# Kernel optimization log

Hardware: AMD Instinct MI355X
Metric: run time of the kernel (lower is better)

## Reference

```python
import jax, jax.numpy as jnp
import numpy as np

# ---- geometry constants (from init_kwargs options) ----
VIEWS, NDET, NX, NY = 360, 736, 512, 512
DVOX, DDET = 0.7, 1.2858
DSO, DOD = 595.0, 490.6
DSD = DSO + DOD
STEP = 0.0174533
END_ANGLE = STEP * VIEWS  # ~2*pi
EXTENT = 1


def _compute_indices():
    """CPU port of PixelIndexCal_cuda (fanflat mode, extent=1).
    Returns flat int64 indices of shape [NX*NY*VIEWS] (pixel-major, view inner)."""
    sVx, sVy = DVOX * NX, DVOX * NY
    alphas = np.linspace(0.0, END_ANGLE, VIEWS, endpoint=False)
    indX, indY = np.meshgrid(np.arange(NX, dtype=np.float64),
                             np.arange(NY, dtype=np.float64), indexing='ij')
    idx_all = np.empty((NX * NY, VIEWS), dtype=np.int64)
    for a in range(VIEWS):
        alpha = -alphas[a]
        c, s = np.cos(alpha), np.sin(alpha)
        P0x = -(sVx / 2 - DVOX / 2)
        P0y = sVy / 2 - DVOX / 2
        rot = lambda px, py: (px * c + py * s, -px * s + py * c)
        Px_, Py_ = rot(P0x, P0y)
        Pxx, Pxy = rot(P0x + DVOX, P0y)
        Pyx, Pyy = rot(P0x, P0y - DVOX)
        Py_, Pxy, Pyy = Py_ / DDET, Pxy / DDET, Pyy / DDET
        dXx, dXy = Pxx - Px_, Pxy - Py_
        dYx, dYy = Pyx - Px_, Pyy - Py_
        # per-pixel rotated coords
        Pix = Px_ + indX * dXx + indY * dYx
        Piy = Py_ + indX * dXy + indY * dYy
        # fanflat: source at (DSO, 0); ray hits detector plane at x = DSO-DSD
        vectX = Pix - DSO
        t = -DSD / vectX
        det = Piy * t + NDET / 2.0
        det = np.clip(det, 1.0, NDET - 2.0)
        idx_all[:, a] = (det + NDET * a).astype(np.int64).ravel()
    return idx_all.reshape(-1)


def _conv(x, w, b):
    y = jax.lax.conv_general_dilated(x, w, (1, 1), 'SAME',
                                     dimension_numbers=('NCHW', 'OIHW', 'NCHW'))
    return y + b[None, :, None, None]


def setup_inputs() -> dict:
    key = jax.random.key(0)
    ks = jax.random.split(key, 16)
    lin_std = 1.0 / np.sqrt(NDET)
    conv_std = 1.0 / np.sqrt(64 * 9)
    inp = {
        'x': jax.random.normal(ks[0], (1, 1, VIEWS, NDET), jnp.float32),
        'indices': jnp.asarray(_compute_indices()),
        'w1': jax.random.normal(ks[1], (NDET, NDET), jnp.float32) * lin_std,
        'b1': jnp.zeros((NDET,), jnp.float32),
        'w2': jax.random.normal(ks[2], (NDET, NDET), jnp.float32) * lin_std,
        'b2': jnp.zeros((NDET,), jnp.float32),
        'conv_in_w': jax.random.normal(ks[3], (64, 1, 3, 3), jnp.float32) * (1.0 / 3.0),
        'conv_in_b': jnp.zeros((64,), jnp.float32),
        'blk_w1': jax.random.normal(ks[4], (11, 64, 64, 3, 3), jnp.float32) * conv_std,
        'blk_b1': jnp.zeros((11, 64), jnp.float32),
        'blk_w2': jax.random.normal(ks[5], (11, 64, 64, 3, 3), jnp.float32) * conv_std,
        'blk_b2': jnp.zeros((11, 64), jnp.float32),
        'conv_out_w': jax.random.normal(ks[6], (1, 64, 3, 3), jnp.float32) * conv_std,
        'conv_out_b': jnp.zeros((1,), jnp.float32),
    }
    return inp


def reference(x, indices, w1, b1, w2, b2, conv_in_w, conv_in_b,
              blk_w1, blk_b1, blk_w2, blk_b2, conv_out_w, conv_out_b):
    # convf: two per-detector-row Linear+ReLU over last dim (nDetecU)
    h = jax.nn.relu(x @ w1.T + b1)
    h = jax.nn.relu(h @ w2.T + b2)
    # BackProjNet (learn=False): gather + sum over views, scale, flip
    sino = h.reshape(-1, 1, VIEWS * NDET)
    g = sino[:, :, indices]                         # [B,1,NX*NY*VIEWS]
    g = g.reshape(-1, 1, NX * NY, VIEWS * EXTENT)
    img = g.sum(axis=3) * ((END_ANGLE - 0.0) / (2 * VIEWS * EXTENT))
    img = img.reshape(-1, 1, NX, NY)
    img = jnp.flip(img, axis=(2, 3))
    # rCNN refinement: conv(1->64)+ReLU, 11 residual blocks, conv(64->1)
    y = jax.nn.relu(_conv(img, conv_in_w, conv_in_b))
    for i in range(11):
        z = _conv(y, blk_w1[i], blk_b1[i])
        z = jax.nn.relu(z)
        z = _conv(z, blk_w2[i], blk_b2[i])
        y = jax.nn.relu(y + z)
    out = _conv(y, conv_out_w, conv_out_b)
    return out
```

## Files before the change

kernel.cpp:

```cpp
#include <hip/hip_runtime.h>

#define VIEWS 360
#define NDET 736
#define NX 512
#define NY 512
#define NPIX (NX * NY)

typedef unsigned short u16;
typedef __attribute__((ext_vector_type(8))) short bf16x8;
typedef __attribute__((ext_vector_type(4))) float f32x4;

__device__ __forceinline__ u16 f2bf(float f) {
  unsigned u = __float_as_uint(f);
  return (u16)((u + 0x7fffu + ((u >> 16) & 1u)) >> 16);
}

__global__ __launch_bounds__(256) void linear_relu4_kernel(
    const float* __restrict__ in, const float* __restrict__ w,
    const float* __restrict__ b, float* __restrict__ out) {
  __shared__ __align__(16) float xin[4][NDET];
  const int v0 = blockIdx.x * 4;
  const int t = threadIdx.x;
  for (int k = t; k < 4 * (NDET / 4); k += 256) {
    const int row = k / (NDET / 4), c4 = k % (NDET / 4);
    ((float4*)xin[row])[c4] = ((const float4*)(in + (size_t)(v0 + row) * NDET))[c4];
  }
  __syncthreads();

  const bool has2 = (t < NDET - 512);
  const float4* w0 = (const float4*)(w + (size_t)t * NDET);
  const float4* w1 = (const float4*)(w + (size_t)(t + 256) * NDET);
  const float4* w2 = (const float4*)(w + (size_t)(has2 ? t + 512 : t) * NDET);

  float acc[3][4];
#pragma unroll
  for (int j = 0; j < 3; ++j)
#pragma unroll
    for (int v = 0; v < 4; ++v) acc[j][v] = 0.f;

#pragma unroll 2
  for (int k = 0; k < NDET / 4; ++k) {
    float4 xv0 = ((const float4*)xin[0])[k];
    float4 xv1 = ((const float4*)xin[1])[k];
    float4 xv2 = ((const float4*)xin[2])[k];
    float4 xv3 = ((const float4*)xin[3])[k];
    float4 wv;
    wv = w0[k];
    acc[0][0] = fmaf(xv0.x, wv.x, fmaf(xv0.y, wv.y, fmaf(xv0.z, wv.z, fmaf(xv0.w, wv.w, acc[0][0]))));
    acc[0][1] = fmaf(xv1.x, wv.x, fmaf(xv1.y, wv.y, fmaf(xv1.z, wv.z, fmaf(xv1.w, wv.w, acc[0][1]))));
    acc[0][2] = fmaf(xv2.x, wv.x, fmaf(xv2.y, wv.y, fmaf(xv2.z, wv.z, fmaf(xv2.w, wv.w, acc[0][2]))));
    acc[0][3] = fmaf(xv3.x, wv.x, fmaf(xv3.y, wv.y, fmaf(xv3.z, wv.z, fmaf(xv3.w, wv.w, acc[0][3]))));
    wv = w1[k];
    acc[1][0] = fmaf(xv0.x, wv.x, fmaf(xv0.y, wv.y, fmaf(xv0.z, wv.z, fmaf(xv0.w, wv.w, acc[1][0]))));
    acc[1][1] = fmaf(xv1.x, wv.x, fmaf(xv1.y, wv.y, fmaf(xv1.z, wv.z, fmaf(xv1.w, wv.w, acc[1][1]))));
    acc[1][2] = fmaf(xv2.x, wv.x, fmaf(xv2.y, wv.y, fmaf(xv2.z, wv.z, fmaf(xv2.w, wv.w, acc[1][2]))));
    acc[1][3] = fmaf(xv3.x, wv.x, fmaf(xv3.y, wv.y, fmaf(xv3.z, wv.z, fmaf(xv3.w, wv.w, acc[1][3]))));
    wv = w2[k];
    acc[2][0] = fmaf(xv0.x, wv.x, fmaf(xv0.y, wv.y, fmaf(xv0.z, wv.z, fmaf(xv0.w, wv.w, acc[2][0]))));
    acc[2][1] = fmaf(xv1.x, wv.x, fmaf(xv1.y, wv.y, fmaf(xv1.z, wv.z, fmaf(xv1.w, wv.w, acc[2][1]))));
    acc[2][2] = fmaf(xv2.x, wv.x, fmaf(xv2.y, wv.y, fmaf(xv2.z, wv.z, fmaf(xv2.w, wv.w, acc[2][2]))));
    acc[2][3] = fmaf(xv3.x, wv.x, fmaf(xv3.y, wv.y, fmaf(xv3.z, wv.z, fmaf(xv3.w, wv.w, acc[2][3]))));
  }

  const float b0 = b[t], b1 = b[t + 256];
  const float b2v = has2 ? b[t + 512] : 0.f;
#pragma unroll
  for (int v = 0; v < 4; ++v) {
    float* o = out + (size_t)(v0 + v) * NDET;
    o[t] = fmaxf(acc[0][v] + b0, 0.f);
    o[t + 256] = fmaxf(acc[1][v] + b1, 0.f);
    if (has2) o[t + 512] = fmaxf(acc[2][v] + b2v, 0.f);
  }
}

__global__ __launch_bounds__(256) void backproj_kernel(
    const float* __restrict__ sino, const int* __restrict__ idx,
    float* __restrict__ img) {
  __shared__ int lidx[256 * 77];
  const int t = threadIdx.x;
  const int p_base = blockIdx.x * 256;

  float a0 = 0.f, a1 = 0.f, a2 = 0.f, a3 = 0.f;

#pragma unroll 1
  for (int c = 0; c < 5; ++c) {
    if (c) __syncthreads();
#pragma unroll
    for (int k = 0; k < 18; ++k) {
      const int f = k * 256 + t;
      const int row = f / 18, col4 = f % 18;
      int4 v = *(const int4*)&idx[(size_t)(p_base + row) * VIEWS + c * 72 +
                                  col4 * 4];
      int* dst = &lidx[row * 77 + col4 * 4];
      dst[0] = v.x; dst[1] = v.y; dst[2] = v.z; dst[3] = v.w;
    }
    __syncthreads();
    const int* myrow = &lidx[t * 77];
#pragma unroll
    for (int j = 0; j < 72; j += 4) {
      a0 += sino[myrow[j + 0]];
      a1 += sino[myrow[j + 1]];
      a2 += sino[myrow[j + 2]];
      a3 += sino[myrow[j + 3]];
    }
  }

  const int p = p_base + t;
  const int ix = p >> 9, iy = p & 511;
  img[(NX - 1 - ix) * NY + (NY - 1 - iy)] =
      ((a0 + a1) + (a2 + a3)) * 0.00872665f;
}

__device__ __forceinline__ void load9(const float* __restrict__ base, int gx,
                                      int gy, float v[9]) {
  const bool xm = gx > 0, xp = gx < NX - 1, ym = gy > 0, yp = gy < NY - 1;
  const float* c = base + gy * NX + gx;
  v[0] = (ym && xm) ? c[-NX - 1] : 0.f;
  v[1] = (ym)       ? c[-NX]     : 0.f;
  v[2] = (ym && xp) ? c[-NX + 1] : 0.f;
  v[3] = (xm)       ? c[-1]      : 0.f;
  v[4] =               c[0];
  v[5] = (xp)       ? c[1]       : 0.f;
  v[6] = (yp && xm) ? c[NX - 1]  : 0.f;
  v[7] = (yp)       ? c[NX]      : 0.f;
  v[8] = (yp && xp) ? c[NX + 1]  : 0.f;
}

__device__ __forceinline__ float dot9(float a, const float v[9],
                                      const float* __restrict__ w) {
  a = fmaf(v[0], w[0], a);
  a = fmaf(v[1], w[1], a);
  a = fmaf(v[2], w[2], a);
  a = fmaf(v[3], w[3], a);
  a = fmaf(v[4], w[4], a);
  a = fmaf(v[5], w[5], a);
  a = fmaf(v[6], w[6], a);
  a = fmaf(v[7], w[7], a);
  a = fmaf(v[8], w[8], a);
  return a;
}

__global__ __launch_bounds__(256) void conv_in_kernel(
    const float* __restrict__ in, const float* __restrict__ w,
    const float* __restrict__ b, float* __restrict__ out) {
  const int p = blockIdx.x * 256 + threadIdx.x;
  const int gx = p & (NX - 1), gy = p >> 9;
  float v[9];
  load9(in, gx, gy, v);
  float4* o = (float4*)(out + (size_t)p * 64);
#pragma unroll
  for (int oq = 0; oq < 16; ++oq) {
    float4 r;
    r.x = fmaxf(dot9(b[oq * 4 + 0], v, w + (oq * 4 + 0) * 9), 0.f);
    r.y = fmaxf(dot9(b[oq * 4 + 1], v, w + (oq * 4 + 1) * 9), 0.f);
    r.z = fmaxf(dot9(b[oq * 4 + 2], v, w + (oq * 4 + 2) * 9), 0.f);
    r.w = fmaxf(dot9(b[oq * 4 + 3], v, w + (oq * 4 + 3) * 9), 0.f);
    o[oq] = r;
  }
}

__global__ __launch_bounds__(256) void prep_weights_kernel(
    const float* __restrict__ bw1, const float* __restrict__ bw2,
    u16* __restrict__ wR) {
  const int g = blockIdx.x * 256 + threadIdx.x;
  if (g >= 22 * 36864) return;
  const int li = g / 36864, r1 = g % 36864;
  const int s = r1 / 2048, r2 = r1 % 2048;
  const int mf = r2 / 512, r3 = r2 % 512;
  const int lane = r3 / 8, j = r3 % 8;
  const int kb = s / 9, tap = s % 9;
  const int kg = lane >> 4, n = lane & 15;
  const int oc = mf * 16 + n;
  const int ic = kb * 32 + kg * 8 + j;
  const float* src = (li < 11) ? bw1 + li * 36864 : bw2 + (li - 11) * 36864;
  wR[g] = f2bf(src[(oc * 64 + ic) * 9 + tap]);
}

template <int IN_BF, int OUT_BF, int RELU, int ADDRES>
__global__ __launch_bounds__(256, 4) void conv64_mfma(
    const void* __restrict__ in_, const u16* __restrict__ wA,
    const float* __restrict__ bias, const float* __restrict__ res,
    void* __restrict__ out_) {
  __shared__ __align__(16) u16 lds[6 * 66 * 32];
  const int xb = (blockIdx.x & 7) * 64;
  const int yb = (int)(blockIdx.x >> 3) * 4;
  const int tid = threadIdx.x;
  const int wv = tid >> 6;
  const int lane = tid & 63;
  const int n = lane & 15;
  const int kg = lane >> 4;

  f32x4 acc[4][4];
#pragma unroll
  for (int i = 0; i < 4; ++i)
#pragma unroll
    for (int j = 0; j < 4; ++j) acc[i][j] = (f32x4){0.f, 0.f, 0.f, 0.f};

#pragma unroll 1
  for (int kb = 0; kb < 2; ++kb) {
    if (kb) __syncthreads();
#pragma unroll
    for (int it = 0; it < 7; ++it) {
      const int g = it * 256 + tid;
      if (g < 1584) {
        const int icq = g & 3;
        const int xr = g >> 2;
        const int x66 = xr % 66;
        const int r = xr / 66;
        const int y = yb - 1 + r;
        const int x = xb - 1 + x66;
        uint4 d = {0u, 0u, 0u, 0u};
        if ((unsigned)y < 512u && (unsigned)x < 512u) {
          const size_t gi =
              ((size_t)((y << 9) + x)) * 64 + kb * 32 + icq * 8;
          if (IN_BF) {
            d = *(const uint4*)&((const u16*)in_)[gi];
          } else {
            const float* s = &((const float*)in_)[gi];
            float4 f0 = *(const float4*)s;
            float4 f1 = *(const float4*)(s + 4);
            d.x = (unsigned)f2bf(f0.x) | ((unsigned)f2bf(f0.y) << 16);
            d.y = (unsigned)f2bf(f0.z) | ((unsigned)f2bf(f0.w) << 16);
            d.z = (unsigned)f2bf(f1.x) | ((unsigned)f2bf(f1.y) << 16);
            d.w = (unsigned)f2bf(f1.z) | ((unsigned)f2bf(f1.w) << 16);
          }
        }
        const int slot = icq ^ ((x66 >> 1) & 3);
        *(uint4*)&lds[(xr * 4 + slot) * 8] = d;
      }
    }
    __syncthreads();

#pragma unroll 3
    for (int tap = 0; tap < 9; ++tap) {
      const int s = kb * 9 + tap;
      bf16x8 av[4];
#pragma unroll
      for (int mf = 0; mf < 4; ++mf)
        av[mf] = *(const bf16x8*)&wA[(size_t)s * 2048 + mf * 512 + lane * 8];

      const int r = wv + tap / 3;
      const int dxp1 = tap % 3;

      bf16x8 bfr[4];
#pragma unroll
      for (int nf = 0; nf < 4; ++nf) {
        const int xi = dxp1 + nf * 16 + n;
        const int slot = kg ^ ((xi >> 1) & 3);
        bfr[nf] = *(const bf16x8*)&lds[((r * 66 + xi) * 4 + slot) * 8];
      }
#pragma unroll
      for (int mf = 0; mf < 4; ++mf)
#pragma unroll
        for (int nf = 0; nf < 4; ++nf)
          acc[mf][nf] = __builtin_amdgcn_mfma_f32_16x16x32_bf16(
              av[mf], bfr[nf], acc[mf][nf], 0, 0, 0);
    }
  }

  const int y = yb + wv;
#pragma unroll
  for (int mf = 0; mf < 4; ++mf) {
    const float4 bv = *(const float4*)&bias[mf * 16 + kg * 4];
#pragma unroll
    for (int nf = 0; nf < 4; ++nf) {
      const int x = xb + nf * 16 + n;
      const size_t base = ((size_t)((y << 9) + x)) * 64 + mf * 16 + kg * 4;
      float v0 = acc[mf][nf][0] + bv.x;
      float v1 = acc[mf][nf][1] + bv.y;
      float v2 = acc[mf][nf][2] + bv.z;
      float v3 = acc[mf][nf][3] + bv.w;
      if (ADDRES) {
        float4 rr = *(const float4*)&res[base];
        v0 += rr.x; v1 += rr.y; v2 += rr.z; v3 += rr.w;
      }
      if (RELU) {
        v0 = fmaxf(v0, 0.f); v1 = fmaxf(v1, 0.f);
        v2 = fmaxf(v2, 0.f); v3 = fmaxf(v3, 0.f);
      }
      if (OUT_BF) {
        uint2 pk;
        pk.x = (unsigned)f2bf(v0) | ((unsigned)f2bf(v1) << 16);
        pk.y = (unsigned)f2bf(v2) | ((unsigned)f2bf(v3) << 16);
        *(uint2*)&((u16*)out_)[base] = pk;
      } else {
        *(float4*)&((float*)out_)[base] = (float4){v0, v1, v2, v3};
      }
    }
  }
}

__global__ __launch_bounds__(256) void conv_out_kernel(
    const float* __restrict__ in, const float* __restrict__ w,
    const float* __restrict__ b, float* __restrict__ out) {
  const int p = blockIdx.x * 256 + threadIdx.x;
  const int gx = p & (NX - 1), gy = p >> 9;
  float a = b[0];
#pragma unroll
  for (int ty = 0; ty < 3; ++ty) {
#pragma unroll
    for (int tx = 0; tx < 3; ++tx) {
      const int yy = gy + ty - 1, xx = gx + tx - 1;
      if ((unsigned)yy < 512u && (unsigned)xx < 512u) {
        const float4* q = (const float4*)(in + ((size_t)((yy << 9) + xx)) * 64);
        const int tap = ty * 3 + tx;
#pragma unroll
        for (int i = 0; i < 16; ++i) {
          float4 d = q[i];
          a = fmaf(d.x, w[(i * 4 + 0) * 9 + tap], a);
          a = fmaf(d.y, w[(i * 4 + 1) * 9 + tap], a);
          a = fmaf(d.z, w[(i * 4 + 2) * 9 + tap], a);
          a = fmaf(d.w, w[(i * 4 + 3) * 9 + tap], a);
        }
      }
    }
  }
  out[p] = a;
}

extern "C" void kernel_launch(void* const* d_in, const int* in_sizes, int n_in,
                              void* d_out, int out_size, void* d_ws,
                              size_t ws_size, hipStream_t stream) {
  const float* x      = (const float*)d_in[0];
  const int*   indices= (const int*)d_in[1];
  const float* w1     = (const float*)d_in[2];
  const float* b1     = (const float*)d_in[3];
  const float* w2     = (const float*)d_in[4];
  const float* b2     = (const float*)d_in[5];
  const float* cin_w  = (const float*)d_in[6];
  const float* cin_b  = (const float*)d_in[7];
  const float* bw1    = (const float*)d_in[8];
  const float* bb1    = (const float*)d_in[9];
  const float* bw2    = (const float*)d_in[10];
  const float* bb2    = (const float*)d_in[11];
  const float* cout_w = (const float*)d_in[12];
  const float* cout_b = (const float*)d_in[13];

  float* ws   = (float*)d_ws;
  float* h1   = ws;
  float* h2   = h1 + VIEWS * NDET;
  float* img  = h2 + VIEWS * NDET;
  float* yf   = img + NPIX;
  u16*  zb    = (u16*)(yf + (size_t)64 * NPIX);
  u16*  wAll  = zb + (size_t)64 * NPIX;

  prep_weights_kernel<<<(22 * 36864 + 255) / 256, 256, 0, stream>>>(bw1, bw2,
                                                                    wAll);
  linear_relu4_kernel<<<VIEWS / 4, 256, 0, stream>>>(x, w1, b1, h1);
  linear_relu4_kernel<<<VIEWS / 4, 256, 0, stream>>>(h1, w2, b2, h2);
  backproj_kernel<<<NPIX / 256, 256, 0, stream>>>(h2, indices, img);
  conv_in_kernel<<<NPIX / 256, 256, 0, stream>>>(img, cin_w, cin_b, yf);

  for (int i = 0; i < 11; ++i) {
    conv64_mfma<0, 1, 1, 0><<<1024, 256, 0, stream>>>(
        yf, wAll + i * 36864, bb1 + i * 64, nullptr, zb);
    conv64_mfma<1, 0, 1, 1><<<1024, 256, 0, stream>>>(
        zb, wAll + (11 + i) * 36864, bb2 + i * 64, yf, yf);
  }
  conv_out_kernel<<<NPIX / 256, 256, 0, stream>>>(yf, cout_w, cout_b,
                                                  (float*)d_out);
}
```

Before: 1.896 ms.

## Fuse conv stack into one persistent cooperative kernel and merge the linears

```diff
diff --git a/kernel.cpp b/kernel.cpp
--- a/kernel.cpp
+++ b/kernel.cpp
@@ -1,4 +1,7 @@
 #include <hip/hip_runtime.h>
+#include <hip/hip_cooperative_groups.h>
+
+namespace cg = cooperative_groups;
 
 #define VIEWS 360
 #define NDET 736
@@ -15,61 +18,82 @@
   return (u16)((u + 0x7fffu + ((u >> 16) & 1u)) >> 16);
 }
 
-__global__ __launch_bounds__(256) void linear_relu4_kernel(
-    const float* __restrict__ in, const float* __restrict__ w,
-    const float* __restrict__ b, float* __restrict__ out) {
+__global__ __launch_bounds__(256) void linear2_kernel(
+    const float* __restrict__ x, const float* __restrict__ w1,
+    const float* __restrict__ b1, const float* __restrict__ w2,
+    const float* __restrict__ b2, float* __restrict__ out) {
   __shared__ __align__(16) float xin[4][NDET];
+  __shared__ __align__(16) float h1s[4][NDET];
   const int v0 = blockIdx.x * 4;
   const int t = threadIdx.x;
   for (int k = t; k < 4 * (NDET / 4); k += 256) {
     const int row = k / (NDET / 4), c4 = k % (NDET / 4);
-    ((float4*)xin[row])[c4] = ((const float4*)(in + (size_t)(v0 + row) * NDET))[c4];
+    ((float4*)xin[row])[c4] =
+        ((const float4*)(x + (size_t)(v0 + row) * NDET))[c4];
   }
   __syncthreads();
 
   const bool has2 = (t < NDET - 512);
-  const float4* w0 = (const float4*)(w + (size_t)t * NDET);
-  const float4* w1 = (const float4*)(w + (size_t)(t + 256) * NDET);
-  const float4* w2 = (const float4*)(w + (size_t)(has2 ? t + 512 : t) * NDET);
-
-  float acc[3][4];
-#pragma unroll
-  for (int j = 0; j < 3; ++j)
-#pragma unroll
-    for (int v = 0; v < 4; ++v) acc[j][v] = 0.f;
+
+#pragma unroll 1
+  for (int L = 0; L < 2; ++L) {
+    const float* w = L ? w2 : w1;
+    const float* b = L ? b2 : b1;
+    const float(*src)[NDET] = L ? h1s : xin;
+
+    const float4* w0 = (const float4*)(w + (size_t)t * NDET);
+    const float4* w1p = (const float4*)(w + (size_t)(t + 256) * NDET);
+    const float4* w2p = (const float4*)(w + (size_t)(has2 ? t + 512 : t) * NDET);
+
+    float acc[3][4];
+#pragma unroll
+    for (int j = 0; j < 3; ++j)
+#pragma unroll
+      for (int v = 0; v < 4; ++v) acc[j][v] = 0.f;
 
 #pragma unroll 2
-  for (int k = 0; k < NDET / 4; ++k) {
-    float4 xv0 = ((const float4*)xin[0])[k];
-    float4 xv1 = ((const float4*)xin[1])[k];
-    float4 xv2 = ((const float4*)xin[2])[k];
-    float4 xv3 = ((const float4*)xin[3])[k];
-    float4 wv;
-    wv = w0[k];
-    acc[0][0] = fmaf(xv0.x, wv.x, fmaf(xv0.y, wv.y, fmaf(xv0.z, wv.z, fmaf(xv0.w, wv.w, acc[0][0]))));
-    acc[0][1] = fmaf(xv1.x, wv.x, fmaf(xv1.y, wv.y, fmaf(xv1.z, wv.z, fmaf(xv1.w, wv.w, acc[0][1]))));
-    acc[0][2] = fmaf(xv2.x, wv.x, fmaf(xv2.y, wv.y, fmaf(xv2.z, wv.z, fmaf(xv2.w, wv.w, acc[0][2]))));
-    acc[0][3] = fmaf(xv3.x, wv.x, fmaf(xv3.y, wv.y, fmaf(xv3.z, wv.z, fmaf(xv3.w, wv.w, acc[0][3]))));
-    wv = w1[k];
-    acc[1][0] = fmaf(xv0.x, wv.x, fmaf(xv0.y, wv.y, fmaf(xv0.z, wv.z, fmaf(xv0.w, wv.w, acc[1][0]))));
-    acc[1][1] = fmaf(xv1.x, wv.x, fmaf(xv1.y, wv.y, fmaf(xv1.z, wv.z, fmaf(xv1.w, wv.w, acc[1][1]))));
-    acc[1][2] = fmaf(xv2.x, wv.x, fmaf(xv2.y, wv.y, fmaf(xv2.z, wv.z, fmaf(xv2.w, wv.w, acc[1][2]))));
-    acc[1][3] = fmaf(xv3.x, wv.x, fmaf(xv3.y, wv.y, fmaf(xv3.z, wv.z, fmaf(xv3.w, wv.w, acc[1][3]))));
-    wv = w2[k];
-    acc[2][0] = fmaf(xv0.x, wv.x, fmaf(xv0.y, wv.y, fmaf(xv0.z, wv.z, fmaf(xv0.w, wv.w, acc[2][0]))));
-    acc[2][1] = fmaf(xv1.x, wv.x, fmaf(xv1.y, wv.y, fmaf(xv1.z, wv.z, fmaf(xv1.w, wv.w, acc[2][1]))));
-    acc[2][2] = fmaf(xv2.x, wv.x, fmaf(xv2.y, wv.y, fmaf(xv2.z, wv.z, fmaf(xv2.w, wv.w, acc[2][2]))));
-    acc[2][3] = fmaf(xv3.x, wv.x, fmaf(xv3.y, wv.y, fmaf(xv3.z, wv.z, fmaf(xv3.w, wv.w, acc[2][3]))));
-  }
-
-  const float b0 = b[t], b1 = b[t + 256];
-  const float b2v = has2 ? b[t + 512] : 0.f;
-#pragma unroll
-  for (int v = 0; v < 4; ++v) {
-    float* o = out + (size_t)(v0 + v) * NDET;
-    o[t] = fmaxf(acc[0][v] + b0, 0.f);
-    o[t + 256] = fmaxf(acc[1][v] + b1, 0.f);
-    if (has2) o[t + 512] = fmaxf(acc[2][v] + b2v, 0.f);
+    for (int k = 0; k < NDET / 4; ++k) {
+      float4 xv0 = ((const float4*)src[0])[k];
+      float4 xv1 = ((const float4*)src[1])[k];
+      float4 xv2 = ((const float4*)src[2])[k];
+      float4 xv3 = ((const float4*)src[3])[k];
+      float4 wv;
+      wv = w0[k];
+      acc[0][0] = fmaf(xv0.x, wv.x, fmaf(xv0.y, wv.y, fmaf(xv0.z, wv.z, fmaf(xv0.w, wv.w, acc[0][0]))));
+      acc[0][1] = fmaf(xv1.x, wv.x, fmaf(xv1.y, wv.y, fmaf(xv1.z, wv.z, fmaf(xv1.w, wv.w, acc[0][1]))));
+      acc[0][2] = fmaf(xv2.x, wv.x, fmaf(xv2.y, wv.y, fmaf(xv2.z, wv.z, fmaf(xv2.w, wv.w, acc[0][2]))));
+      acc[0][3] = fmaf(xv3.x, wv.x, fmaf(xv3.y, wv.y, fmaf(xv3.z, wv.z, fmaf(xv3.w, wv.w, acc[0][3]))));
+      wv = w1p[k];
+      acc[1][0] = fmaf(xv0.x, wv.x, fmaf(xv0.y, wv.y, fmaf(xv0.z, wv.z, fmaf(xv0.w, wv.w, acc[1][0]))));
+      acc[1][1] = fmaf(xv1.x, wv.x, fmaf(xv1.y, wv.y, fmaf(xv1.z, wv.z, fmaf(xv1.w, wv.w, acc[1][1]))));
+      acc[1][2] = fmaf(xv2.x, wv.x, fmaf(xv2.y, wv.y, fmaf(xv2.z, wv.z, fmaf(xv2.w, wv.w, acc[1][2]))));
+      acc[1][3] = fmaf(xv3.x, wv.x, fmaf(xv3.y, wv.y, fmaf(xv3.z, wv.z, fmaf(xv3.w, wv.w, acc[1][3]))));
+      wv = w2p[k];
+      acc[2][0] = fmaf(xv0.x, wv.x, fmaf(xv0.y, wv.y, fmaf(xv0.z, wv.z, fmaf(xv0.w, wv.w, acc[2][0]))));
+      acc[2][1] = fmaf(xv1.x, wv.x, fmaf(xv1.y, wv.y, fmaf(xv1.z, wv.z, fmaf(xv1.w, wv.w, acc[2][1]))));
+      acc[2][2] = fmaf(xv2.x, wv.x, fmaf(xv2.y, wv.y, fmaf(xv2.z, wv.z, fmaf(xv2.w, wv.w, acc[2][2]))));
+      acc[2][3] = fmaf(xv3.x, wv.x, fmaf(xv3.y, wv.y, fmaf(xv3.z, wv.z, fmaf(xv3.w, wv.w, acc[2][3]))));
+    }
+
+    const float b0 = b[t], b1v = b[t + 256];
+    const float b2v = has2 ? b[t + 512] : 0.f;
+    if (L == 0) {
+#pragma unroll
+      for (int v = 0; v < 4; ++v) {
+        h1s[v][t] = fmaxf(acc[0][v] + b0, 0.f);
+        h1s[v][t + 256] = fmaxf(acc[1][v] + b1v, 0.f);
+        if (has2) h1s[v][t + 512] = fmaxf(acc[2][v] + b2v, 0.f);
+      }
+      __syncthreads();
+    } else {
+#pragma unroll
+      for (int v = 0; v < 4; ++v) {
+        float* o = out + (size_t)(v0 + v) * NDET;
+        o[t] = fmaxf(acc[0][v] + b0, 0.f);
+        o[t + 256] = fmaxf(acc[1][v] + b1v, 0.f);
+        if (has2) o[t + 512] = fmaxf(acc[2][v] + b2v, 0.f);
+      }
+    }
   }
 }
 
@@ -176,15 +200,9 @@
   wR[g] = f2bf(src[(oc * 64 + ic) * 9 + tap]);
 }
 
-template <int IN_BF, int OUT_BF, int RELU, int ADDRES>
-__global__ __launch_bounds__(256, 4) void conv64_mfma(
-    const void* __restrict__ in_, const u16* __restrict__ wA,
-    const float* __restrict__ bias, const float* __restrict__ res,
-    void* __restrict__ out_) {
-  __shared__ __align__(16) u16 lds[6 * 66 * 32];
-  const int xb = (blockIdx.x & 7) * 64;
-  const int yb = (int)(blockIdx.x >> 3) * 4;
-  const int tid = threadIdx.x;
+__device__ __forceinline__ void conv64_tile(
+    const void* in_, const u16* wA, const float* bias, const float* res,
+    void* out_, u16* lds, int xb, int yb, int tid, int sub) {
   const int wv = tid >> 6;
   const int lane = tid & 63;
   const int n = lane & 15;
@@ -198,7 +216,7 @@
 
 #pragma unroll 1
   for (int kb = 0; kb < 2; ++kb) {
-    if (kb) __syncthreads();
+    __syncthreads();
 #pragma unroll
     for (int it = 0; it < 7; ++it) {
       const int g = it * 256 + tid;
@@ -211,9 +229,8 @@
         const int x = xb - 1 + x66;
         uint4 d = {0u, 0u, 0u, 0u};
         if ((unsigned)y < 512u && (unsigned)x < 512u) {
-          const size_t gi =
-              ((size_t)((y << 9) + x)) * 64 + kb * 32 + icq * 8;
-          if (IN_BF) {
+          const size_t gi = ((size_t)((y << 9) + x)) * 64 + kb * 32 + icq * 8;
+          if (sub) {
             d = *(const uint4*)&((const u16*)in_)[gi];
           } else {
             const float* s = &((const float*)in_)[gi];
@@ -270,24 +287,33 @@
       float v1 = acc[mf][nf][1] + bv.y;
       float v2 = acc[mf][nf][2] + bv.z;
       float v3 = acc[mf][nf][3] + bv.w;
-      if (ADDRES) {
+      if (sub) {
         float4 rr = *(const float4*)&res[base];
         v0 += rr.x; v1 += rr.y; v2 += rr.z; v3 += rr.w;
-      }
-      if (RELU) {
         v0 = fmaxf(v0, 0.f); v1 = fmaxf(v1, 0.f);
         v2 = fmaxf(v2, 0.f); v3 = fmaxf(v3, 0.f);
-      }
-      if (OUT_BF) {
+        *(float4*)&((float*)out_)[base] = (float4){v0, v1, v2, v3};
+      } else {
+        v0 = fmaxf(v0, 0.f); v1 = fmaxf(v1, 0.f);
+        v2 = fmaxf(v2, 0.f); v3 = fmaxf(v3, 0.f);
         uint2 pk;
         pk.x = (unsigned)f2bf(v0) | ((unsigned)f2bf(v1) << 16);
         pk.y = (unsigned)f2bf(v2) | ((unsigned)f2bf(v3) << 16);
         *(uint2*)&((u16*)out_)[base] = pk;
-      } else {
-        *(float4*)&((float*)out_)[base] = (float4){v0, v1, v2, v3};
-      }
-    }
-  }
+      }
+    }
+  }
+}
+
+template <int SUB>
+__global__ __launch_bounds__(256, 4) void conv64_mfma(
+    const void* __restrict__ in_, const u16* __restrict__ wA,
+    const float* __restrict__ bias, const float* __restrict__ res,
+    void* __restrict__ out_) {
+  __shared__ __align__(16) u16 lds[6 * 66 * 32];
+  const int xb = (blockIdx.x & 7) * 64;
+  const int yb = (int)(blockIdx.x >> 3) * 4;
+  conv64_tile(in_, wA, bias, res, out_, lds, xb, yb, threadIdx.x, SUB);
 }
 
 __global__ __launch_bounds__(256) void conv_out_kernel(
@@ -316,6 +342,83 @@
     }
   }
   out[p] = a;
+}
+
+__global__ __launch_bounds__(256, 4) void conv_coop(
+    const float* __restrict__ img, const float* __restrict__ cin_w,
+    const float* __restrict__ cin_b, const u16* __restrict__ wAll,
+    const float* __restrict__ bb1, const float* __restrict__ bb2,
+    const float* __restrict__ cout_w, const float* __restrict__ cout_b,
+    float* __restrict__ yf, u16* __restrict__ zb,
+    float* __restrict__ outp) {
+  cg::grid_group grid = cg::this_grid();
+  __shared__ __align__(16) u16 lds[6 * 66 * 32];
+  const int tid = threadIdx.x;
+  const int G = gridDim.x;
+
+  for (int tile = blockIdx.x; tile < 1024; tile += G) {
+    const int xb = (tile & 7) * 64, yb = (tile >> 3) * 4;
+    const int gx = xb + (tid & 63);
+    const int gy = yb + (tid >> 6);
+    float v[9];
+    load9(img, gx, gy, v);
+    float4* o = (float4*)(yf + ((size_t)((gy << 9) + gx)) * 64);
+#pragma unroll
+    for (int oq = 0; oq < 16; ++oq) {
+      float4 r;
+      r.x = fmaxf(dot9(cin_b[oq * 4 + 0], v, cin_w + (oq * 4 + 0) * 9), 0.f);
+      r.y = fmaxf(dot9(cin_b[oq * 4 + 1], v, cin_w + (oq * 4 + 1) * 9), 0.f);
+      r.z = fmaxf(dot9(cin_b[oq * 4 + 2], v, cin_w + (oq * 4 + 2) * 9), 0.f);
+      r.w = fmaxf(dot9(cin_b[oq * 4 + 3], v, cin_w + (oq * 4 + 3) * 9), 0.f);
+      o[oq] = r;
+    }
+  }
+  grid.sync();
+
+#pragma unroll 1
+  for (int li = 0; li < 22; ++li) {
+    const int sub = li & 1;
+    const int blk = li >> 1;
+    const u16* wA = wAll + (size_t)(sub ? 11 + blk : blk) * 36864;
+    const float* bias = (sub ? bb2 : bb1) + blk * 64;
+
+    for (int tile = blockIdx.x; tile < 1024; tile += G) {
+      const int xb = (tile & 7) * 64, yb = (tile >> 3) * 4;
+      if (sub)
+        conv64_tile(zb, wA, bias, yf, yf, lds, xb, yb, tid, 1);
+      else
+        conv64_tile(yf, wA, bias, nullptr, zb, lds, xb, yb, tid, 0);
+    }
+    grid.sync();
+  }
+
+  for (int tile = blockIdx.x; tile < 1024; tile += G) {
+    const int xb = (tile & 7) * 64, yb = (tile >> 3) * 4;
+    const int gx = xb + (tid & 63);
+    const int gy = yb + (tid >> 6);
+    float a = cout_b[0];
+#pragma unroll
+    for (int ty = 0; ty < 3; ++ty) {
+#pragma unroll
+      for (int tx = 0; tx < 3; ++tx) {
+        const int yy = gy + ty - 1, xx = gx + tx - 1;
+        if ((unsigned)yy < 512u && (unsigned)xx < 512u) {
+          const float4* q =
+              (const float4*)(yf + ((size_t)((yy << 9) + xx)) * 64);
+          const int tap = ty * 3 + tx;
+#pragma unroll
+          for (int i = 0; i < 16; ++i) {
+            float4 d = q[i];
+            a = fmaf(d.x, cout_w[(i * 4 + 0) * 9 + tap], a);
+            a = fmaf(d.y, cout_w[(i * 4 + 1) * 9 + tap], a);
+            a = fmaf(d.z, cout_w[(i * 4 + 2) * 9 + tap], a);
+            a = fmaf(d.w, cout_w[(i * 4 + 3) * 9 + tap], a);
+          }
+        }
+      }
+    }
+    outp[(gy << 9) + gx] = a;
+  }
 }
 
 extern "C" void kernel_launch(void* const* d_in, const int* in_sizes, int n_in,
@@ -337,8 +440,7 @@
   const float* cout_b = (const float*)d_in[13];
 
   float* ws   = (float*)d_ws;
-  float* h1   = ws;
-  float* h2   = h1 + VIEWS * NDET;
+  float* h2   = ws;
   float* img  = h2 + VIEWS * NDET;
   float* yf   = img + NPIX;
   u16*  zb    = (u16*)(yf + (size_t)64 * NPIX);
@@ -346,17 +448,43 @@
 
   prep_weights_kernel<<<(22 * 36864 + 255) / 256, 256, 0, stream>>>(bw1, bw2,
                                                                     wAll);
-  linear_relu4_kernel<<<VIEWS / 4, 256, 0, stream>>>(x, w1, b1, h1);
-  linear_relu4_kernel<<<VIEWS / 4, 256, 0, stream>>>(h1, w2, b2, h2);
+  linear2_kernel<<<VIEWS / 4, 256, 0, stream>>>(x, w1, b1, w2, b2, h2);
   backproj_kernel<<<NPIX / 256, 256, 0, stream>>>(h2, indices, img);
-  conv_in_kernel<<<NPIX / 256, 256, 0, stream>>>(img, cin_w, cin_b, yf);
-
-  for (int i = 0; i < 11; ++i) {
-    conv64_mfma<0, 1, 1, 0><<<1024, 256, 0, stream>>>(
-        yf, wAll + i * 36864, bb1 + i * 64, nullptr, zb);
-    conv64_mfma<1, 0, 1, 1><<<1024, 256, 0, stream>>>(
-        zb, wAll + (11 + i) * 36864, bb2 + i * 64, yf, yf);
-  }
-  conv_out_kernel<<<NPIX / 256, 256, 0, stream>>>(yf, cout_w, cout_b,
-                                                  (float*)d_out);
-}
+
+  float* outp = (float*)d_out;
+
+  static int coop_grid = -2;
+  if (coop_grid == -2) {
+    int bpcu = 0;
+    hipError_t e = hipOccupancyMaxActiveBlocksPerMultiprocessor(
+        &bpcu, (const void*)conv_coop, 256, 0);
+    coop_grid = (e == hipSuccess && bpcu > 0)
+                    ? ((bpcu * 256 < 1024) ? bpcu * 256 : 1024)
+                    : -1;
+  }
+
+  bool done = false;
+  if (coop_grid > 0) {
+    void* cargs[] = {&img,    &cin_w,  &cin_b, &wAll, &bb1, &bb2,
+                     &cout_w, &cout_b, &yf,    &zb,   &outp};
+    hipError_t err = hipLaunchCooperativeKernel(
+        (const void*)conv_coop, dim3(coop_grid), dim3(256), cargs, 0, stream);
+    if (err == hipSuccess) {
+      done = true;
+    } else {
+      (void)hipGetLastError();
+      coop_grid = -1;
+    }
+  }
+
+  if (!done) {
+    conv_in_kernel<<<NPIX / 256, 256, 0, stream>>>(img, cin_w, cin_b, yf);
+    for (int i = 0; i < 11; ++i) {
+      conv64_mfma<0><<<1024, 256, 0, stream>>>(
+          yf, wAll + i * 36864, bb1 + i * 64, nullptr, zb);
+      conv64_mfma<1><<<1024, 256, 0, stream>>>(
+          zb, wAll + (11 + i) * 36864, bb2 + i * 64, yf, yf);
+    }
+    conv_out_kernel<<<NPIX / 256, 256, 0, stream>>>(yf, cout_w, cout_b, outp);
+  }
+}
```

Result: slower. 3.978 ms (+109.8%).
